# Kernel optimization log

Hardware: AMD Instinct MI355X
Metric: run time of the kernel (lower is better)

Reference implementation:

```python
import jax, jax.numpy as jnp
import numpy as np

B, S, H, KV, D = 1, 2048, 32, 8, 128
HID = H * D
SINK, WIN, POOL = 128, 1024, 100
TAU = 1.0


def setup_inputs() -> dict:
    key = jax.random.key(0)
    ks = jax.random.split(key, 12)
    init = lambda k, shape: jax.random.normal(k, shape, jnp.float32) * 0.02
    return dict(
        hidden_states=jax.random.normal(ks[0], (B, S, HID), jnp.float32),
        Wq=init(ks[1], (HID, HID)),
        Wk=init(ks[2], (HID, KV * D)),
        Wv=init(ks[3], (HID, KV * D)),
        Wo=init(ks[4], (HID, HID)),
        fe1_w=init(ks[5], (D, 8 * D)), fe1_b=jnp.zeros((8 * D,), jnp.float32),
        fe2_w=init(ks[6], (8 * D, 2 * D)), fe2_b=jnp.zeros((2 * D,), jnp.float32),
        r1_w=init(ks[7], (2 * D, 4 * D)), r1_b=jnp.zeros((4 * D,), jnp.float32),
        r2_w=init(ks[8], (4 * D, D)), r2_b=jnp.zeros((D,), jnp.float32),
        r3_w=init(ks[9], (D, 1)), r3_b=jnp.zeros((1,), jnp.float32),
        router_noise=jax.random.uniform(ks[10], (B, 1), jnp.float32),
    )


def _rope(x):
    # x: [B,S,h,D]; non-interleaved (rotate-half) RoPE, base 10000
    half = D // 2
    inv_freq = 1.0 / (10000.0 ** (jnp.arange(0, D, 2, dtype=jnp.float32) / D))
    t = jnp.arange(S, dtype=jnp.float32)
    freqs = jnp.outer(t, inv_freq)  # [S, half]
    cos = jnp.cos(freqs)[None, :, None, :]
    sin = jnp.sin(freqs)[None, :, None, :]
    x1, x2 = x[..., :half], x[..., half:]
    return jnp.concatenate([x1 * cos - x2 * sin, x2 * cos + x1 * sin], axis=-1)


def reference(hidden_states, Wq, Wk, Wv, Wo, fe1_w, fe1_b, fe2_w, fe2_b,
              r1_w, r1_b, r2_w, r2_b, r3_w, r3_b, router_noise):
    q = (hidden_states @ Wq).reshape(B, S, H, D)
    k = (hidden_states @ Wk).reshape(B, S, KV, D)
    v = (hidden_states @ Wv).reshape(B, S, KV, D)
    q = _rope(q)
    k = _rope(k)
    # GQA: repeat kv heads
    kr = jnp.repeat(k, H // KV, axis=2)
    vr = jnp.repeat(v, H // KV, axis=2)
    scale = 1.0 / jnp.sqrt(jnp.float32(D))
    scores = jnp.einsum('bshd,bthd->bhst', q, kr) * scale  # [B,H,S,S]
    i = jnp.arange(S)[:, None]
    j = jnp.arange(S)[None, :]
    causal = j <= i
    # sink tokens + sliding window (streaming-LLM pattern)
    stream = causal & ((j < SINK) | (j > i - WIN))
    neg = jnp.float32(-1e30)
    p_full = jax.nn.softmax(jnp.where(causal, scores, neg), axis=-1)
    p_strm = jax.nn.softmax(jnp.where(stream, scores, neg), axis=-1)
    o_full = jnp.einsum('bhst,bthd->bshd', p_full, vr)
    o_strm = jnp.einsum('bhst,bthd->bshd', p_strm, vr)
    # Router: ctx_q pooling over first/last POOL query positions -> [B,H,D] -> [B,D]
    pooled = jnp.concatenate([q[:, :POOL], q[:, -POOL:]], axis=1).mean(axis=1)
    feat = pooled.mean(axis=1)  # [B,D]
    h1 = jax.nn.silu(feat @ fe1_w + fe1_b)
    h2 = h1 @ fe2_w + fe2_b
    h3 = jax.nn.silu(h2 @ r1_w + r1_b)
    h4 = jax.nn.silu(h3 @ r2_w + r2_b)
    logits = h4 @ r3_w + r3_b  # [B,1]
    eps = 1e-8
    g = -jnp.log(-jnp.log(router_noise + eps) + eps)
    z_soft = jax.nn.sigmoid((logits + g) / TAU)
    z_hard = (z_soft > 0.5).astype(z_soft.dtype)
    z = z_hard + z_soft - jax.lax.stop_gradient(z_soft)  # straight-through
    mix = z.reshape(B, 1, 1, 1)
    o = mix * o_strm + (1.0 - mix) * o_full  # gate sparse vs full retrieval
    return o.reshape(B, S, HID) @ Wo
```

## Files before the change

kernel.cpp:

```cpp
#include <hip/hip_runtime.h>
#include <hip/hip_bf16.h>

typedef unsigned short u16;
typedef unsigned int u32;
typedef __bf16 bf16x8 __attribute__((ext_vector_type(8)));
typedef float f32x4 __attribute__((ext_vector_type(4)));
typedef unsigned short u16x8 __attribute__((ext_vector_type(8)));

#define S_ 2048
#define H_ 32
#define KV_ 8
#define D_ 128
#define HID_ 4096
#define KVD_ 1024
#define QKVN 6144
#define SINK_ 128
#define WIN_ 1024
#define POOL_ 100
#define KVB 64
#define QB 128

__device__ __forceinline__ u16 f2bf(float f) {
  union { float f; u32 u; } v; v.f = f;
  u32 r = v.u + 0x7FFFu + ((v.u >> 16) & 1u);
  return (u16)(r >> 16);
}
__device__ __forceinline__ float bf2f(u16 h) {
  union { u32 u; float f; } v; v.u = ((u32)h) << 16;
  return v.f;
}
__device__ __forceinline__ void glds16(const void* g, void* l) {
  __builtin_amdgcn_global_load_lds((__attribute__((address_space(1))) void*)g,
                                   (__attribute__((address_space(3))) void*)l, 16, 0, 0);
}

__device__ __forceinline__ void tr64(const float* __restrict__ W, u16* __restrict__ Wt,
                                     int K, int N, int nt, int kt, int tid, u16 T[64][66]) {
  const int r = tid >> 4, c4 = tid & 15;
#pragma unroll
  for (int p = 0; p < 4; ++p) {
    int row = p * 16 + r;
    float4 v = *(const float4*)&W[(size_t)(kt * 64 + row) * N + nt * 64 + c4 * 4];
    T[row][c4 * 4 + 0] = f2bf(v.x);
    T[row][c4 * 4 + 1] = f2bf(v.y);
    T[row][c4 * 4 + 2] = f2bf(v.z);
    T[row][c4 * 4 + 3] = f2bf(v.w);
  }
  __syncthreads();
  const int n = tid >> 3, c8 = tid & 7;
#pragma unroll
  for (int p = 0; p < 2; ++p) {
    int row = p * 32 + n;
    u16x8 o;
#pragma unroll
    for (int i = 0; i < 8; ++i) o[i] = T[c8 * 8 + i][row];
    *(u16x8*)&Wt[(size_t)(nt * 64 + row) * K + kt * 64 + c8 * 8] = o;
  }
}

__global__ __launch_bounds__(256) void k_prep(const float* __restrict__ hs, u16* __restrict__ hsb,
                                              const float* __restrict__ Wq, const float* __restrict__ Wk,
                                              const float* __restrict__ Wv, const float* __restrict__ Wo,
                                              u16* __restrict__ wqkv, u16* __restrict__ wot,
                                              float* __restrict__ cosT, float* __restrict__ sinT) {
  __shared__ u16 T[64][66];
  const int b = blockIdx.x, tid = threadIdx.x;
  if (b < 8192) {
    int i = b * 256 + tid;
    float4 v = ((const float4*)hs)[i];
    union { u16 s[4]; unsigned long long ll; } o;
    o.s[0] = f2bf(v.x); o.s[1] = f2bf(v.y); o.s[2] = f2bf(v.z); o.s[3] = f2bf(v.w);
    ((unsigned long long*)hsb)[i] = o.ll;
  } else if (b < 12288) {
    int id = b - 8192;
    tr64(Wq, wqkv, HID_, HID_, id % 64, id / 64, tid, T);
  } else if (b < 13312) {
    int id = b - 12288;
    tr64(Wk, wqkv + (size_t)4096 * HID_, HID_, KVD_, id % 16, id / 16, tid, T);
  } else if (b < 14336) {
    int id = b - 13312;
    tr64(Wv, wqkv + (size_t)5120 * HID_, HID_, KVD_, id % 16, id / 16, tid, T);
  } else if (b < 18432) {
    int id = b - 14336;
    tr64(Wo, wot, HID_, HID_, id % 64, id / 64, tid, T);
  } else {
    int idx = (b - 18432) * 256 + tid;
    int s = idx >> 6, i = idx & 63;
    float inv = powf(10000.f, -(float)i * (1.f / 64.f));
    float ang = (float)s * inv;
    cosT[idx] = cosf(ang);
    sinT[idx] = sinf(ang);
  }
}

__global__ __launch_bounds__(256) void k_pos(u16* __restrict__ qkv, u16* __restrict__ kro,
                                             u16* __restrict__ vt,
                                             const float* __restrict__ cosT, const float* __restrict__ sinT) {
  __shared__ u16 T[32][33];
  const int b = blockIdx.x, tid = threadIdx.x;
  if (b < 16384) {
    int idx = b * 256 + tid;
    int i = idx & 63, h = (idx >> 6) & 31, s = idx >> 11;
    size_t base = (size_t)s * QKVN + h * D_ + i;
    float x1 = bf2f(qkv[base]), x2 = bf2f(qkv[base + 64]);
    float cs = cosT[(s << 6) + i], sn = sinT[(s << 6) + i];
    qkv[base] = f2bf(x1 * cs - x2 * sn);
    qkv[base + 64] = f2bf(x2 * cs + x1 * sn);
  } else if (b < 20480) {
    int idx = (b - 16384) * 256 + tid;
    int i = idx & 63, kv = (idx >> 6) & 7, s = idx >> 9;
    float x1 = bf2f(qkv[(size_t)s * QKVN + 4096 + kv * D_ + i]);
    float x2 = bf2f(qkv[(size_t)s * QKVN + 4096 + kv * D_ + i + 64]);
    float cs = cosT[(s << 6) + i], sn = sinT[(s << 6) + i];
    size_t ob = (size_t)kv * S_ * D_ + (size_t)s * D_ + i;
    kro[ob] = f2bf(x1 * cs - x2 * sn);
    kro[ob + 64] = f2bf(x2 * cs + x1 * sn);
  } else {
    int id = b - 20480;
    int st = id & 63, dt = (id >> 6) & 3, kv = id >> 8;
    int c = tid & 31, r0 = tid >> 5;
#pragma unroll
    for (int p = 0; p < 4; ++p) {
      int r = r0 + p * 8;
      T[r][c] = qkv[(size_t)(st * 32 + r) * QKVN + 5120 + kv * D_ + dt * 32 + c];
    }
    __syncthreads();
#pragma unroll
    for (int p = 0; p < 4; ++p) {
      int r = r0 + p * 8;
      vt[(size_t)kv * D_ * S_ + (size_t)(dt * 32 + r) * S_ + st * 32 + c] = T[c][r];
    }
  }
}

__global__ void k_feat(const u16* __restrict__ q, float* __restrict__ feat) {
  int d = blockIdx.x, tid = threadIdx.x;
  float p = 0.f;
  for (int idx = tid; idx < 2 * POOL_ * H_; idx += 256) {
    int pos = idx >> 5, hh = idx & 31;
    int s = pos < POOL_ ? pos : (S_ - 2 * POOL_) + pos;
    p += bf2f(q[(size_t)s * QKVN + hh * D_ + d]);
  }
#pragma unroll
  for (int m = 1; m < 64; m <<= 1) p += __shfl_xor(p, m);
  __shared__ float red[4];
  if ((tid & 63) == 0) red[tid >> 6] = p;
  __syncthreads();
  if (tid == 0) feat[d] = (red[0] + red[1] + red[2] + red[3]) * (1.f / (2 * POOL_ * H_));
}

__global__ __launch_bounds__(256) void k_r1(const float* __restrict__ feat, const float* __restrict__ w,
                                            const float* __restrict__ b, float* __restrict__ h1) {
  __shared__ float fs[128];
  int tid = threadIdx.x;
  if (tid < 128) fs[tid] = feat[tid];
  __syncthreads();
  int o = blockIdx.x * 256 + tid;
  float a = b[o];
#pragma unroll 16
  for (int kk = 0; kk < 128; ++kk) a += fs[kk] * w[kk * 1024 + o];
  h1[o] = a / (1.f + expf(-a));
}
__global__ __launch_bounds__(256) void k_r2(const float* __restrict__ h1, const float* __restrict__ w,
                                            float* __restrict__ h2p) {
  __shared__ float hs[64];
  int tid = threadIdx.x, b = blockIdx.x;
  if (tid < 64) hs[tid] = h1[b * 64 + tid];
  __syncthreads();
  const float* wb = w + (size_t)b * 64 * 256 + tid;
  float p = 0.f;
#pragma unroll 16
  for (int kk = 0; kk < 64; ++kk) p += hs[kk] * wb[(size_t)kk * 256];
  h2p[b * 256 + tid] = p;
}
__global__ __launch_bounds__(256) void k_r3(const float* __restrict__ h2p, const float* __restrict__ b2,
                                            const float* __restrict__ w, const float* __restrict__ b3,
                                            float* __restrict__ h3) {
  __shared__ float h2s[256];
  int tid = threadIdx.x;
  float s = b2[tid];
#pragma unroll
  for (int j = 0; j < 16; ++j) s += h2p[j * 256 + tid];
  h2s[tid] = s;
  __syncthreads();
  int o = blockIdx.x * 256 + tid;
  float a = b3[o];
#pragma unroll 16
  for (int kk = 0; kk < 256; ++kk) a += h2s[kk] * w[kk * 512 + o];
  h3[o] = a / (1.f + expf(-a));
}
__global__ __launch_bounds__(256) void k_r45(const float* __restrict__ h3, const float* __restrict__ w4,
                                             const float* __restrict__ b4, const float* __restrict__ w5,
                                             const float* __restrict__ b5, const float* __restrict__ noise,
                                             float* __restrict__ mix) {
  __shared__ float h3s[512];
  __shared__ float hp[256];
  int tid = threadIdx.x;
  h3s[tid] = h3[tid];
  h3s[tid + 256] = h3[tid + 256];
  __syncthreads();
  int t = tid & 127, half = tid >> 7;
  float a = half ? 0.f : b4[t];
  const float* wcol = w4 + (size_t)(half << 8) * 128 + t;
  const float* hbase = h3s + (half << 8);
#pragma unroll 16
  for (int i = 0; i < 256; ++i) a += hbase[i] * wcol[(size_t)i * 128];
  hp[tid] = a;
  __syncthreads();
  if (tid < 128) {
    float v = hp[tid] + hp[tid + 128];
    float h4 = v / (1.f + expf(-v));
    hp[tid] = h4 * w5[tid];
  }
  __syncthreads();
  if (tid < 64) {
    float s = hp[tid] + hp[tid + 64];
#pragma unroll
    for (int m = 32; m >= 1; m >>= 1) s += __shfl_down(s, m);
    if (tid == 0) {
      float logits = s + b5[0];
      float u = noise[0];
      float g = -logf(-logf(u + 1e-8f) + 1e-8f);
      float zs = 1.f / (1.f + expf(-(logits + g)));
      mix[0] = zs > 0.5f ? 1.f : 0.f;
    }
  }
}

template <int MFRAG, int NFRAG>
__device__ __forceinline__ void stage_u(const u16* __restrict__ A, const u16* __restrict__ Bt,
                                        u16* buf, int m0, int n0, int K, int kg, int unit, int tid) {
  constexpr int AU = MFRAG / 2;
  constexpr int BM = MFRAG * 32;
  if (unit < AU) {
    int cell = unit * 512 + tid;
    int row = cell >> 3, c = cell & 7;
    glds16(A + (size_t)(m0 + row) * K + kg + ((c ^ (row & 7)) * 8),
           buf + ((size_t)(unit * 512 + (tid & ~63))) * 8);
  } else {
    int cell = (unit - AU) * 512 + tid;
    int row = cell >> 3, c = cell & 7;
    glds16(Bt + (size_t)(n0 + row) * K + kg + ((c ^ (row & 7)) * 8),
           buf + (size_t)BM * 64 + ((size_t)((unit - AU) * 512 + (tid & ~63))) * 8);
  }
}

template <int MFRAG, int NFRAG, int OUTF32>
__global__ __launch_bounds__(512, 1) void gemm_dp(const u16* __restrict__ A, const u16* __restrict__ Bt,
                                                  void* __restrict__ C, int M, int N, int K, int NTN) {
  constexpr int BM = MFRAG * 32;
  constexpr int BN = NFRAG * 64;
  constexpr int NH = NFRAG / 2;
  constexpr int U = MFRAG / 2 + NFRAG;
  static_assert(U == 8 || U == 6, "stage schedule assumes 6 or 8 units");
  constexpr int TE = (BM + BN) * 64;
  __shared__ __align__(16) u16 lds[2 * TE];
  const int tid = threadIdx.x, w = tid >> 6, ln = tid & 63;
  const int lr = ln & 15, lk = ln >> 4;
  const int wr = w >> 2, wc = w & 3;
  const int nwg = gridDim.x, cpx = nwg >> 3;
  const int wg = (blockIdx.x & 7) * cpx + (blockIdx.x >> 3);
  const int m0 = (wg / NTN) * BM, n0 = (wg % NTN) * BN;
  f32x4 acc[MFRAG][NFRAG];
#pragma unroll
  for (int i = 0; i < MFRAG; ++i)
#pragma unroll
    for (int j = 0; j < NFRAG; ++j) acc[i][j] = (f32x4){0.f, 0.f, 0.f, 0.f};
  const int nt = K / 64;

  auto ldA = [&](const u16* buf, bf16x8* af, int kh) {
#pragma unroll
    for (int mf = 0; mf < MFRAG; ++mf) {
      int row = wr * (MFRAG * 16) + mf * 16 + lr;
      af[mf] = *(const bf16x8*)&buf[row * 64 + (((kh * 4 + lk) ^ (row & 7)) * 8)];
    }
  };
  auto ldB = [&](const u16* buf, bf16x8* bp, int kh, int nh) {
#pragma unroll
    for (int nf = 0; nf < NH; ++nf) {
      int brow = wc * (NFRAG * 16) + (nh * NH + nf) * 16 + lr;
      bp[nf] = *(const bf16x8*)&buf[BM * 64 + brow * 64 + (((kh * 4 + lk) ^ (brow & 7)) * 8)];
    }
  };
  auto MMA = [&](const bf16x8* af, const bf16x8* bp, int nh) {
    __builtin_amdgcn_s_setprio(1);
#pragma unroll
    for (int mf = 0; mf < MFRAG; ++mf)
#pragma unroll
      for (int nf = 0; nf < NH; ++nf)
        acc[mf][nh * NH + nf] =
            __builtin_amdgcn_mfma_f32_16x16x32_bf16(af[mf], bp[nf], acc[mf][nh * NH + nf], 0, 0, 0);
    __builtin_amdgcn_s_setprio(0);
  };

#pragma unroll
  for (int i = 0; i < U; ++i) stage_u<MFRAG, NFRAG>(A, Bt, lds, m0, n0, K, 0, i, tid);
  stage_u<MFRAG, NFRAG>(A, Bt, lds + TE, m0, n0, K, 64, 0, tid);
  stage_u<MFRAG, NFRAG>(A, Bt, lds + TE, m0, n0, K, 64, 1, tid);
  asm volatile("s_waitcnt vmcnt(2)" ::: "memory");
  asm volatile("s_barrier" ::: "memory");
  bf16x8 afA[MFRAG], afB[MFRAG], b0[NH], b1[NH];
  ldA(lds, afA, 0);
  ldB(lds, b0, 0, 0);

  for (int t = 0; t < nt; ++t) {
    const u16* cb = lds + (t & 1) * TE;
    u16* nb = lds + ((t + 1) & 1) * TE;
    const bool hn = (t + 1 < nt);
    const int kn = (t + 1) * 64;
    MMA(afA, b0, 0);
    ldB(cb, b1, 0, 1);
    if (hn) {
      stage_u<MFRAG, NFRAG>(A, Bt, nb, m0, n0, K, kn, 2, tid);
      stage_u<MFRAG, NFRAG>(A, Bt, nb, m0, n0, K, kn, 3, tid);
    }
    MMA(afA, b1, 1);
    ldA(cb, afB, 1);
    ldB(cb, b0, 1, 0);
    if (hn) {
      stage_u<MFRAG, NFRAG>(A, Bt, nb, m0, n0, K, kn, 4, tid);
      stage_u<MFRAG, NFRAG>(A, Bt, nb, m0, n0, K, kn, 5, tid);
    }
    MMA(afB, b0, 0);
    ldB(cb, b1, 1, 1);
    if (hn && U == 8) {
      stage_u<MFRAG, NFRAG>(A, Bt, nb, m0, n0, K, kn, 6, tid);
      stage_u<MFRAG, NFRAG>(A, Bt, nb, m0, n0, K, kn, 7, tid);
    }
    MMA(afB, b1, 1);
    asm volatile("s_barrier" ::: "memory");
    if (hn) {
      if (t + 2 < nt) {
        stage_u<MFRAG, NFRAG>(A, Bt, (u16*)cb, m0, n0, K, (t + 2) * 64, 0, tid);
        stage_u<MFRAG, NFRAG>(A, Bt, (u16*)cb, m0, n0, K, (t + 2) * 64, 1, tid);
        asm volatile("s_waitcnt vmcnt(2)" ::: "memory");
      } else {
        asm volatile("s_waitcnt vmcnt(0)" ::: "memory");
      }
      asm volatile("s_barrier" ::: "memory");
      ldA(nb, afA, 0);
      ldB(nb, b0, 0, 0);
    }
  }
#pragma unroll
  for (int mf = 0; mf < MFRAG; ++mf) {
    int row = m0 + wr * (MFRAG * 16) + mf * 16 + lk * 4;
#pragma unroll
    for (int nf = 0; nf < NFRAG; ++nf) {
      int col = n0 + wc * (NFRAG * 16) + nf * 16 + lr;
#pragma unroll
      for (int jj = 0; jj < 4; ++jj) {
        float v = acc[mf][nf][jj];
        if (OUTF32) ((float*)C)[(size_t)(row + jj) * N + col] = v;
        else ((u16*)C)[(size_t)(row + jj) * N + col] = f2bf(v);
      }
    }
  }
}

__global__ __launch_bounds__(512) void k_attn(const u16* __restrict__ q, const u16* __restrict__ kr,
                                              const u16* __restrict__ vt, u16* __restrict__ o,
                                              const float* __restrict__ mixp, int qs) {
  __shared__ __align__(16) u16 Ks[2][KVB * 128];
  __shared__ __align__(16) u16 Vs[2][128 * KVB];
  __shared__ __align__(16) u16 Ps[8][16 * KVB];
  const int tid = threadIdx.x, w = tid >> 6, ln = tid & 63;
  const int lr = ln & 15, lk = ln >> 4;
  const int bid = blockIdx.x;
  const int qblk = (S_ / QB - 1) - (bid >> 5);
  const int h = bid & 31, kv = h >> 2;
  const bool strm = (*mixp) > 0.5f;
  const int q0 = qblk * QB;
  const int qrow = q0 + w * 16 + lr;
  bf16x8 qf[4];
#pragma unroll
  for (int c = 0; c < 4; ++c)
    qf[c] = *(const bf16x8*)(q + (size_t)qrow * qs + h * D_ + c * 32 + lk * 8);
  f32x4 oacc[8];
#pragma unroll
  for (int c = 0; c < 8; ++c) oacc[c] = (f32x4){0.f, 0.f, 0.f, 0.f};
  float mrun[4], lrun[4];
#pragma unroll
  for (int j = 0; j < 4; ++j) { mrun[j] = -1e30f; lrun[j] = 0.f; }
  const u16* kbase = kr + (size_t)kv * S_ * D_;
  const u16* vbase = vt + (size_t)kv * D_ * S_;
  const int qg0 = q0 + w * 16 + lk * 4;
  const float scale = 0.08838834764831845f;
  const int ntl = 2 * qblk + 2;

  auto stage = [&](int kt, int b) {
    const int kb0 = kt * KVB;
#pragma unroll
    for (int c = 0; c < 2; ++c) {
      int r0 = c * 32 + w * 4;
      int rg = r0 + (ln >> 4);
      int cg = (ln & 15) ^ (rg & 7);
      glds16(kbase + (size_t)(kb0 + rg) * D_ + cg * 8, &Ks[b][r0 * 128]);
    }
#pragma unroll
    for (int c = 0; c < 2; ++c) {
      int r0 = c * 64 + w * 8;
      int rg = r0 + (ln >> 3);
      int cg = (ln & 7) ^ (rg & 7);
      glds16(vbase + (size_t)rg * S_ + kb0 + cg * 8, &Vs[b][r0 * KVB]);
    }
  };
  auto nxt = [&](int k) {
    ++k;
    if (strm)
      while (k < ntl && k * KVB >= SINK_ && k * KVB + KVB - 1 + WIN_ <= q0) ++k;
    return k;
  };

  int kt = 0, buf = 0;
  stage(0, 0);
  int ktn = nxt(0);
  while (kt < ntl) {
    const bool hn = (ktn < ntl);
    if (hn) {
      stage(ktn, buf ^ 1);
      asm volatile("s_waitcnt vmcnt(4)" ::: "memory");
    } else {
      asm volatile("s_waitcnt vmcnt(0)" ::: "memory");
    }
    asm volatile("s_barrier" ::: "memory");
    const int kb0 = kt * KVB;
    const u16* ks = Ks[buf];
    const u16* vs = Vs[buf];
    f32x4 sg[4];
#pragma unroll
    for (int g = 0; g < 4; ++g) sg[g] = (f32x4){0.f, 0.f, 0.f, 0.f};
    __builtin_amdgcn_s_setprio(1);
#pragma unroll
    for (int g = 0; g < 4; ++g) {
      int krow = g * 16 + lr;
      int sw = krow & 7;
#pragma unroll
      for (int c = 0; c < 4; ++c) {
        bf16x8 kf = *(const bf16x8*)&ks[krow * 128 + (((c * 4 + lk) ^ sw) * 8)];
        sg[g] = __builtin_amdgcn_mfma_f32_16x16x32_bf16(qf[c], kf, sg[g], 0, 0, 0);
      }
    }
    __builtin_amdgcn_s_setprio(0);
    const bool diag = (kt >= 2 * qblk);
    const bool needm = diag ||
        (strm && !(kb0 + KVB <= SINK_ || kb0 >= q0 + QB - WIN_));
    if (needm) {
#pragma unroll
      for (int g = 0; g < 4; ++g) {
        int kg = kb0 + g * 16 + lr;
#pragma unroll
        for (int j = 0; j < 4; ++j) {
          int qi = qg0 + j;
          float v = sg[g][j] * scale;
          bool ok = (kg <= qi) && (!strm || kg < SINK_ || kg > qi - WIN_);
          sg[g][j] = ok ? v : -1e30f;
        }
      }
    } else {
#pragma unroll
      for (int g = 0; g < 4; ++g)
#pragma unroll
        for (int j = 0; j < 4; ++j) sg[g][j] *= scale;
    }
    float rmax[4];
#pragma unroll
    for (int j = 0; j < 4; ++j)
      rmax[j] = fmaxf(fmaxf(sg[0][j], sg[1][j]), fmaxf(sg[2][j], sg[3][j]));
#pragma unroll
    for (int m2 = 1; m2 < 16; m2 <<= 1)
#pragma unroll
      for (int j = 0; j < 4; ++j) rmax[j] = fmaxf(rmax[j], __shfl_xor(rmax[j], m2));
    float dmax = rmax[0] - mrun[0];
#pragma unroll
    for (int j = 1; j < 4; ++j) dmax = fmaxf(dmax, rmax[j] - mrun[j]);
    if (!__all(dmax <= 8.f)) {
      float corr[4];
#pragma unroll
      for (int j = 0; j < 4; ++j) {
        float mn = fmaxf(mrun[j], rmax[j]);
        corr[j] = __expf(mrun[j] - mn);
        mrun[j] = mn;
        lrun[j] *= corr[j];
      }
#pragma unroll
      for (int c = 0; c < 8; ++c) {
        f32x4 t2 = oacc[c];
        t2[0] *= corr[0]; t2[1] *= corr[1]; t2[2] *= corr[2]; t2[3] *= corr[3];
        oacc[c] = t2;
      }
    }
    float rsum[4] = {0.f, 0.f, 0.f, 0.f};
#pragma unroll
    for (int g = 0; g < 4; ++g)
#pragma unroll
      for (int j = 0; j < 4; ++j) {
        float p = __expf(sg[g][j] - mrun[j]);
        sg[g][j] = p;
        rsum[j] += p;
      }
#pragma unroll
    for (int m2 = 1; m2 < 16; m2 <<= 1)
#pragma unroll
      for (int j = 0; j < 4; ++j) rsum[j] += __shfl_xor(rsum[j], m2);
#pragma unroll
    for (int j = 0; j < 4; ++j) lrun[j] += rsum[j];
#pragma unroll
    for (int g = 0; g < 4; ++g) {
      int col = g * 16 + lr;
      int c16 = col >> 3;
#pragma unroll
      for (int j = 0; j < 4; ++j) {
        int row = lk * 4 + j;
        Ps[w][row * KVB + ((c16 ^ (row & 7)) * 8) + (col & 7)] = f2bf(sg[g][j]);
      }
    }
    __builtin_amdgcn_s_setprio(1);
#pragma unroll
    for (int half = 0; half < 2; ++half) {
      bf16x8 pf = *(const bf16x8*)&Ps[w][lr * KVB + (((half * 4 + lk) ^ (lr & 7)) * 8)];
#pragma unroll
      for (int cc = 0; cc < 8; ++cc) {
        int vrow = cc * 16 + lr;
        bf16x8 vf = *(const bf16x8*)&vs[vrow * KVB + (((half * 4 + lk) ^ (vrow & 7)) * 8)];
        oacc[cc] = __builtin_amdgcn_mfma_f32_16x16x32_bf16(pf, vf, oacc[cc], 0, 0, 0);
      }
    }
    __builtin_amdgcn_s_setprio(0);
    asm volatile("s_barrier" ::: "memory");
    kt = ktn;
    ktn = nxt(ktn);
    buf ^= 1;
  }
#pragma unroll
  for (int cc = 0; cc < 8; ++cc)
#pragma unroll
    for (int j = 0; j < 4; ++j) {
      float ov = oacc[cc][j] / lrun[j];
      o[(size_t)(qg0 + j) * HID_ + h * D_ + cc * 16 + lr] = f2bf(ov);
    }
}

extern "C" void kernel_launch(void* const* d_in, const int* in_sizes, int n_in,
                              void* d_out, int out_size, void* d_ws, size_t ws_size,
                              hipStream_t stream) {
  const float* hs = (const float*)d_in[0];
  const float* Wq = (const float*)d_in[1];
  const float* Wk = (const float*)d_in[2];
  const float* Wv = (const float*)d_in[3];
  const float* Wo = (const float*)d_in[4];
  const float* fe1_w = (const float*)d_in[5];
  const float* fe1_b = (const float*)d_in[6];
  const float* fe2_w = (const float*)d_in[7];
  const float* fe2_b = (const float*)d_in[8];
  const float* r1_w = (const float*)d_in[9];
  const float* r1_b = (const float*)d_in[10];
  const float* r2_w = (const float*)d_in[11];
  const float* r2_b = (const float*)d_in[12];
  const float* r3_w = (const float*)d_in[13];
  const float* r3_b = (const float*)d_in[14];
  const float* noise = (const float*)d_in[15];

  char* ws = (char*)d_ws;
  size_t off = 0;
  auto alloc = [&](size_t b) { char* p = ws + off; off += (b + 255) & ~(size_t)255; return p; };
  u16* hsb = (u16*)alloc((size_t)S_ * HID_ * 2);
  u16* wqkv = (u16*)alloc((size_t)QKVN * HID_ * 2);
  u16* qkvbuf = (u16*)alloc((size_t)S_ * QKVN * 2);
  u16* wot = (u16*)alloc((size_t)HID_ * HID_ * 2);
  u16* krbuf = (u16*)alloc((size_t)S_ * KVD_ * 2);
  u16* vtbuf = (u16*)alloc((size_t)S_ * KVD_ * 2);
  u16* obuf = (u16*)alloc((size_t)S_ * HID_ * 2);
  float* cosT = (float*)alloc((size_t)S_ * 64 * 4);
  float* sinT = (float*)alloc((size_t)S_ * 64 * 4);
  float* feat = (float*)alloc(512);
  float* mix = (float*)alloc(256);
  float* h1buf = (float*)alloc(1024 * 4);
  float* h2p = (float*)alloc(16 * 256 * 4);
  float* h3buf = (float*)alloc(512 * 4);

  k_prep<<<dim3(18944), dim3(256), 0, stream>>>(hs, hsb, Wq, Wk, Wv, Wo, wqkv, wot, cosT, sinT);

  gemm_dp<4, 6, 0><<<dim3(256), dim3(512), 0, stream>>>(hsb, wqkv, (void*)qkvbuf,
                                                        S_, QKVN, HID_, QKVN / 384);

  k_pos<<<dim3(22528), dim3(256), 0, stream>>>(qkvbuf, krbuf, vtbuf, cosT, sinT);

  k_feat<<<dim3(D_), dim3(256), 0, stream>>>(qkvbuf, feat);
  k_r1<<<dim3(4), dim3(256), 0, stream>>>(feat, fe1_w, fe1_b, h1buf);
  k_r2<<<dim3(16), dim3(256), 0, stream>>>(h1buf, fe2_w, h2p);
  k_r3<<<dim3(2), dim3(256), 0, stream>>>(h2p, fe2_b, r1_w, r1_b, h3buf);
  k_r45<<<dim3(1), dim3(256), 0, stream>>>(h3buf, r2_w, r2_b, r3_w, r3_b, noise, mix);

  k_attn<<<dim3((S_ / QB) * H_), dim3(512), 0, stream>>>(qkvbuf, krbuf, vtbuf, obuf, mix, QKVN);

  gemm_dp<4, 4, 1><<<dim3(256), dim3(512), 0, stream>>>(obuf, wot, d_out,
                                                        S_, HID_, HID_, HID_ / 256);
}
```

Measured before the change: 360.2 us.

## Move Wo transpose-convert from prep kernel into attention launch tail blocks

The Wo fp32-to-bf16 transpose moves out of the prep kernel and into 4096 extra blocks appended to the attention grid. Those blocks reuse the K shared-memory buffer as scratch and return early. The goal is to fill idle CUs at the tail of the causal attention, where the work per block is uneven, and so take Wo conversion off the critical path. In exchange, the 512-thread attention launch now carries many small blocks, each using 512 threads and the attention kernel's large shared-memory footprint, which may limit occupancy during those blocks.

Result: no change. 354.2 us (-1.7%).

```diff
diff --git a/kernel.cpp b/kernel.cpp
--- a/kernel.cpp
+++ b/kernel.cpp
@@ -19,6 +19,7 @@
 #define POOL_ 100
 #define KVB 64
 #define QB 128
+#define ATTNB ((S_ / QB) * H_)
 
 __device__ __forceinline__ u16 f2bf(float f) {
   union { float f; u32 u; } v; v.f = f;
@@ -58,10 +59,30 @@
   }
 }
 
+__device__ __forceinline__ void tr64w(const float* __restrict__ W, u16* __restrict__ Wt,
+                                      int K, int N, int nt, int kt, int tid, u16 T[64][66]) {
+  const int r = tid >> 4, c4 = tid & 15;
+#pragma unroll
+  for (int p = 0; p < 2; ++p) {
+    int row = p * 32 + r;
+    float4 v = *(const float4*)&W[(size_t)(kt * 64 + row) * N + nt * 64 + c4 * 4];
+    T[row][c4 * 4 + 0] = f2bf(v.x);
+    T[row][c4 * 4 + 1] = f2bf(v.y);
+    T[row][c4 * 4 + 2] = f2bf(v.z);
+    T[row][c4 * 4 + 3] = f2bf(v.w);
+  }
+  __syncthreads();
+  const int n = tid >> 3, c8 = tid & 7;
+  u16x8 o;
+#pragma unroll
+  for (int i = 0; i < 8; ++i) o[i] = T[c8 * 8 + i][n];
+  *(u16x8*)&Wt[(size_t)(nt * 64 + n) * K + kt * 64 + c8 * 8] = o;
+}
+
 __global__ __launch_bounds__(256) void k_prep(const float* __restrict__ hs, u16* __restrict__ hsb,
                                               const float* __restrict__ Wq, const float* __restrict__ Wk,
-                                              const float* __restrict__ Wv, const float* __restrict__ Wo,
-                                              u16* __restrict__ wqkv, u16* __restrict__ wot,
+                                              const float* __restrict__ Wv,
+                                              u16* __restrict__ wqkv,
                                               float* __restrict__ cosT, float* __restrict__ sinT) {
   __shared__ u16 T[64][66];
   const int b = blockIdx.x, tid = threadIdx.x;
@@ -80,11 +101,8 @@
   } else if (b < 14336) {
     int id = b - 13312;
     tr64(Wv, wqkv + (size_t)5120 * HID_, HID_, KVD_, id % 16, id / 16, tid, T);
-  } else if (b < 18432) {
-    int id = b - 14336;
-    tr64(Wo, wot, HID_, HID_, id % 64, id / 64, tid, T);
   } else {
-    int idx = (b - 18432) * 256 + tid;
+    int idx = (b - 14336) * 256 + tid;
     int s = idx >> 6, i = idx & 63;
     float inv = powf(10000.f, -(float)i * (1.f / 64.f));
     float ang = (float)s * inv;
@@ -360,13 +378,19 @@
 
 __global__ __launch_bounds__(512) void k_attn(const u16* __restrict__ q, const u16* __restrict__ kr,
                                               const u16* __restrict__ vt, u16* __restrict__ o,
-                                              const float* __restrict__ mixp, int qs) {
+                                              const float* __restrict__ mixp, int qs,
+                                              const float* __restrict__ Wo, u16* __restrict__ wot) {
   __shared__ __align__(16) u16 Ks[2][KVB * 128];
   __shared__ __align__(16) u16 Vs[2][128 * KVB];
   __shared__ __align__(16) u16 Ps[8][16 * KVB];
   const int tid = threadIdx.x, w = tid >> 6, ln = tid & 63;
+  const int bid = blockIdx.x;
+  if (bid >= ATTNB) {
+    int id = bid - ATTNB;
+    tr64w(Wo, wot, HID_, HID_, id & 63, id >> 6, tid, (u16(*)[66])(&Ks[0][0]));
+    return;
+  }
   const int lr = ln & 15, lk = ln >> 4;
-  const int bid = blockIdx.x;
   const int qblk = (S_ / QB - 1) - (bid >> 5);
   const int h = bid & 31, kv = h >> 2;
   const bool strm = (*mixp) > 0.5f;
@@ -579,7 +603,7 @@
   float* h2p = (float*)alloc(16 * 256 * 4);
   float* h3buf = (float*)alloc(512 * 4);
 
-  k_prep<<<dim3(18944), dim3(256), 0, stream>>>(hs, hsb, Wq, Wk, Wv, Wo, wqkv, wot, cosT, sinT);
+  k_prep<<<dim3(14848), dim3(256), 0, stream>>>(hs, hsb, Wq, Wk, Wv, wqkv, cosT, sinT);
 
   gemm_dp<4, 6, 0><<<dim3(256), dim3(512), 0, stream>>>(hsb, wqkv, (void*)qkvbuf,
                                                         S_, QKVN, HID_, QKVN / 384);
@@ -592,7 +616,8 @@
   k_r3<<<dim3(2), dim3(256), 0, stream>>>(h2p, fe2_b, r1_w, r1_b, h3buf);
   k_r45<<<dim3(1), dim3(256), 0, stream>>>(h3buf, r2_w, r2_b, r3_w, r3_b, noise, mix);
 
-  k_attn<<<dim3((S_ / QB) * H_), dim3(512), 0, stream>>>(qkvbuf, krbuf, vtbuf, obuf, mix, QKVN);
+  k_attn<<<dim3(ATTNB + 4096), dim3(512), 0, stream>>>(qkvbuf, krbuf, vtbuf, obuf, mix, QKVN,
+                                                       Wo, wot);
 
   gemm_dp<4, 4, 1><<<dim3(256), dim3(512), 0, stream>>>(obuf, wot, d_out,
                                                         S_, HID_, HID_, HID_ / 256);
```
